# Performance work log

Hardware: AMD Instinct MI355X
Metric: run time of the kernel (lower is better)

## Reference

```python
import jax, jax.numpy as jnp
import numpy as np

SIDE_LEN = 128
RESOLUTION = 1.0  # Angstrom per pixel


def setup_inputs() -> dict:
    key = jax.random.key(0)
    k1, k2, k3 = jax.random.split(key, 3)
    B, A = 16, 20000
    # atom xyz coords in Angstrom, spread within the field of view (+/- 63.5 A)
    mol = jax.random.normal(k1, (B, A, 3), dtype=jnp.float32) * 20.0
    # per-atom Gaussian std in [0.5, 1.5) A (strictly positive)
    stds = jax.random.uniform(k2, (A,), dtype=jnp.float32) + 0.5
    # per-atom density (mass) in [0.5, 1.5)
    densities = jax.random.uniform(k3, (A,), dtype=jnp.float32) + 0.5
    return {"mol": mol, "stds": stds, "densities": densities}


def reference(mol, stds, densities):
    # Pixel-center coordinate grid, identical to torch.arange(-x_max, x_max+1e-5, res)
    x_max = (SIDE_LEN - 1) * RESOLUTION / 2
    coord = jnp.arange(-x_max, x_max + 1e-5, RESOLUTION, dtype=jnp.float32)  # (S,)
    var = stds * stds                              # (A,)
    neg_half_inv_var = (-0.5 / var)[None, :, None] # (1,A,1)
    # Separable Gaussian profiles: exp(-(coord - mu)^2 / (2 var))
    dx = coord[None, None, :] - mol[:, :, 0:1]     # (B,A,S) x-offsets
    dy = coord[None, None, :] - mol[:, :, 1:2]     # (B,A,S) y-offsets
    gx = jnp.exp(neg_half_inv_var * dx * dx)       # (B,A,W)
    gy = jnp.exp(neg_half_inv_var * dy * dy)       # (B,A,H)
    coef = densities / (2.0 * jnp.pi * var)        # (A,)
    # img[b,h,w] = sum_a coef_a * gy[b,a,h] * gx[b,a,w]  (batched matmul)
    img = jnp.einsum('bah,baw->bhw', gy * coef[None, :, None], gx)
    return img  # (B, SIDE_LEN, SIDE_LEN)
```

## Files before the change

kernel.cpp:

```cpp
#include <hip/hip_runtime.h>


#define S 128
#define KB 32
#define BLOCK 512
#define LDST 40

typedef _Float16 f16;
typedef _Float16 f16x2 __attribute__((ext_vector_type(2)));
typedef _Float16 f16x8 __attribute__((ext_vector_type(8)));
typedef float floatx4 __attribute__((ext_vector_type(4)));

#if __has_builtin(__builtin_amdgcn_exp2f)
#define FAST_EXP2(x) __builtin_amdgcn_exp2f(x)
#else
#define FAST_EXP2(x) exp2f(x)
#endif
#if __has_builtin(__builtin_amdgcn_rcpf)
#define FAST_RCP(x) __builtin_amdgcn_rcpf(x)
#else
#define FAST_RCP(x) (1.0f / (x))
#endif

__global__ __launch_bounds__(256) void k_prep(const float* __restrict__ stds,
                                              const float* __restrict__ dens,
                                              float* __restrict__ k2,
                                              float* __restrict__ c2, int A) {
    int a = blockIdx.x * 256 + threadIdx.x;
    if (a >= A) return;
    float v  = stds[a] * stds[a];
    float rv = FAST_RCP(v);
    k2[a] = -0.72134752044448f * rv;
    c2[a] = __log2f(dens[a] * 0.15915494309189535f * rv);
}

__global__ __launch_bounds__(BLOCK) void k_proj(
    const float* __restrict__ mol,
    const float* __restrict__ k2,
    const float* __restrict__ c2,
    float* __restrict__ dst,
    int B, int A, int KS, int use_ws)
{
    __shared__ f16 sgx[S * LDST];
    __shared__ f16 sgy[S * LDST];

    const int ks   = blockIdx.x;
    const int b    = blockIdx.y;
    const int tid  = threadIdx.x;
    const int lane = tid & 63;
    const int wav  = tid >> 6;
    const int l15  = lane & 15;
    const int quad = lane >> 4;

    const int per = (A + KS - 1) / KS;
    const int a0 = ks * per;
    const int a1 = min(a0 + per, A);

    floatx4 acc[8];
#pragma unroll
    for (int c = 0; c < 8; ++c) acc[c] = (floatx4){0.f, 0.f, 0.f, 0.f};

    const int kp = (tid & 15) * 2;
    const int pg = tid >> 4;

    for (int base = a0; base < a1; base += KB) {
        const int aA = base + kp, aB = aA + 1;
        float xA = 0.f, yA = 0.f, kA = 0.f, cA = -100000.f;
        float xB = 0.f, yB = 0.f, kB = 0.f, cB = -100000.f;
        if (aA < a1) {
            xA = mol[((size_t)b * A + aA) * 3 + 0];
            yA = mol[((size_t)b * A + aA) * 3 + 1];
            kA = k2[aA];  cA = c2[aA];
        }
        if (aB < a1) {
            xB = mol[((size_t)b * A + aB) * 3 + 0];
            yB = mol[((size_t)b * A + aB) * 3 + 1];
            kB = k2[aB];  cB = c2[aB];
        }

        __syncthreads();
#pragma unroll
        for (int j = 0; j < 4; ++j) {
            const int n = pg + 32 * j;
            const float d = (float)n - 63.5f;
            float dxA = d - xA, dxB = d - xB;
            float exA = FAST_EXP2(dxA * dxA * kA);
            float exB = FAST_EXP2(dxB * dxB * kB);
            *(f16x2*)&sgx[n * LDST + kp] = (f16x2){(f16)exA, (f16)exB};
            float dyA = d - yA, dyB = d - yB;
            float eyA = FAST_EXP2(fmaf(dyA * dyA, kA, cA));
            float eyB = FAST_EXP2(fmaf(dyB * dyB, kB, cB));
            *(f16x2*)&sgy[n * LDST + kp] = (f16x2){(f16)eyA, (f16)eyB};
        }
        __syncthreads();

        f16x8 afr = *(const f16x8*)&sgy[(wav * 16 + l15) * LDST + quad * 8];
#pragma unroll
        for (int c = 0; c < 8; ++c) {
            f16x8 bfr = *(const f16x8*)&sgx[(c * 16 + l15) * LDST + quad * 8];
            acc[c] = __builtin_amdgcn_mfma_f32_16x16x32_f16(afr, bfr, acc[c], 0, 0, 0);
        }
    }

    if (use_ws) {
        float* p = dst + ((size_t)(b * KS + ks)) * (S * S) + wav * 2048;
#pragma unroll
        for (int c = 0; c < 8; ++c)
            *(floatx4*)&p[c * 256 + lane * 4] = acc[c];
    } else {
        const size_t ob = (size_t)b * S * S;
#pragma unroll
        for (int c = 0; c < 8; ++c) {
            const int col = c * 16 + l15;
            const int r0  = wav * 16 + quad * 4;
#pragma unroll
            for (int v = 0; v < 4; ++v)
                atomicAdd(&dst[ob + (size_t)(r0 + v) * S + col], acc[c][v]);
        }
    }
}

__global__ __launch_bounds__(64) void k_reduce(const float* __restrict__ ws,
                                               float* __restrict__ out, int KS) {
    const int ct = blockIdx.x;
    const int w  = blockIdx.y;
    const int b  = blockIdx.z;
    const int t  = threadIdx.x;

    size_t base = ((size_t)b * KS) * (S * S) + w * 2048 + ct * 256 + t * 4;
    floatx4 s0 = {0.f, 0.f, 0.f, 0.f}, s1 = {0.f, 0.f, 0.f, 0.f};
    for (int s = 0; s < KS; s += 2) {
        s0 += *(const floatx4*)&ws[base + (size_t)s * (S * S)];
        s1 += *(const floatx4*)&ws[base + (size_t)(s + 1) * (S * S)];
    }
    floatx4 sum = s0 + s1;

    const int q = t >> 4, l15 = t & 15;
    const int col = ct * 16 + l15;
    const int r0  = w * 16 + q * 4;
#pragma unroll
    for (int v = 0; v < 4; ++v)
        out[((size_t)b * S + (r0 + v)) * S + col] = sum[v];
}

extern "C" void kernel_launch(void* const* d_in, const int* in_sizes, int n_in,
                              void* d_out, int out_size, void* d_ws, size_t ws_size,
                              hipStream_t stream) {
    const float* mol  = (const float*)d_in[0];
    const float* stds = (const float*)d_in[1];
    const float* dens = (const float*)d_in[2];
    float* out = (float*)d_out;

    const int A = in_sizes[1];
    const int B = in_sizes[0] / (A * 3);

    char* ws = (char*)d_ws;
    float* k2 = (float*)ws;
    float* c2 = (float*)(ws + (size_t)A * 4);
    size_t part_off = (((size_t)A * 8) + 255) & ~(size_t)255;
    float* part = (float*)(ws + part_off);

    const size_t img_bytes = (size_t)S * S * 4;
    int KS, use_ws;
    if (ws_size >= part_off + (size_t)64 * B * img_bytes)      { KS = 64; use_ws = 1; }
    else if (ws_size >= part_off + (size_t)32 * B * img_bytes) { KS = 32; use_ws = 1; }
    else                                                       { KS = 32; use_ws = 0; }

    k_prep<<<(A + 255) / 256, 256, 0, stream>>>(stds, dens, k2, c2, A);

    if (!use_ws)
        hipMemsetAsync(d_out, 0, (size_t)out_size * sizeof(float), stream);

    k_proj<<<dim3(KS, B), dim3(BLOCK), 0, stream>>>(
        mol, k2, c2, use_ws ? part : out, B, A, KS, use_ws);

    if (use_ws)
        k_reduce<<<dim3(8, 8, B), dim3(64), 0, stream>>>(part, out, KS);
}
```

Measured before the change: 107.0 us.

## Double-buffer LDS profiles, pack k/c params, fix split at 32 with workspace reduce

Double-buffers the shared gx/gy tiles so each iteration needs only one barrier instead of two. It also packs the per-atom exponent and log-coefficient into one float2 so each atom's parameters come from a single load. The K-split is fixed at 32 slices, and the atomic-add fallback and the workspace-size checks are removed. This cuts block count from 64 to 32 per batch if the workspace previously allowed 64, which lowers parallelism, and it assumes the workspace is always large enough.

```diff
diff --git a/kernel.cpp b/kernel.cpp
--- a/kernel.cpp
+++ b/kernel.cpp
@@ -3,6 +3,7 @@
 
 #define S 128
 #define KB 32
+#define KSPLIT 32
 #define BLOCK 512
 #define LDST 40
 
@@ -24,25 +25,23 @@
 
 __global__ __launch_bounds__(256) void k_prep(const float* __restrict__ stds,
                                               const float* __restrict__ dens,
-                                              float* __restrict__ k2,
-                                              float* __restrict__ c2, int A) {
+                                              float2* __restrict__ kc, int A) {
     int a = blockIdx.x * 256 + threadIdx.x;
     if (a >= A) return;
     float v  = stds[a] * stds[a];
     float rv = FAST_RCP(v);
-    k2[a] = -0.72134752044448f * rv;
-    c2[a] = __log2f(dens[a] * 0.15915494309189535f * rv);
+    kc[a] = make_float2(-0.72134752044448f * rv,
+                        __log2f(dens[a] * 0.15915494309189535f * rv));
 }
 
 __global__ __launch_bounds__(BLOCK) void k_proj(
     const float* __restrict__ mol,
-    const float* __restrict__ k2,
-    const float* __restrict__ c2,
-    float* __restrict__ dst,
-    int B, int A, int KS, int use_ws)
+    const float2* __restrict__ kc,
+    float* __restrict__ part,
+    int B, int A)
 {
-    __shared__ f16 sgx[S * LDST];
-    __shared__ f16 sgy[S * LDST];
+    __shared__ f16 sgx[2][S * LDST];
+    __shared__ f16 sgy[2][S * LDST];
 
     const int ks   = blockIdx.x;
     const int b    = blockIdx.y;
@@ -52,7 +51,7 @@
     const int l15  = lane & 15;
     const int quad = lane >> 4;
 
-    const int per = (A + KS - 1) / KS;
+    const int per = (A + KSPLIT - 1) / KSPLIT;
     const int a0 = ks * per;
     const int a1 = min(a0 + per, A);
 
@@ -63,22 +62,22 @@
     const int kp = (tid & 15) * 2;
     const int pg = tid >> 4;
 
-    for (int base = a0; base < a1; base += KB) {
+    int db = 0;
+    for (int base = a0; base < a1; base += KB, db ^= 1) {
         const int aA = base + kp, aB = aA + 1;
         float xA = 0.f, yA = 0.f, kA = 0.f, cA = -100000.f;
         float xB = 0.f, yB = 0.f, kB = 0.f, cB = -100000.f;
         if (aA < a1) {
             xA = mol[((size_t)b * A + aA) * 3 + 0];
             yA = mol[((size_t)b * A + aA) * 3 + 1];
-            kA = k2[aA];  cA = c2[aA];
+            float2 p = kc[aA];  kA = p.x;  cA = p.y;
         }
         if (aB < a1) {
             xB = mol[((size_t)b * A + aB) * 3 + 0];
             yB = mol[((size_t)b * A + aB) * 3 + 1];
-            kB = k2[aB];  cB = c2[aB];
+            float2 p = kc[aB];  kB = p.x;  cB = p.y;
         }
 
-        __syncthreads();
 #pragma unroll
         for (int j = 0; j < 4; ++j) {
             const int n = pg + 32 * j;
@@ -86,50 +85,38 @@
             float dxA = d - xA, dxB = d - xB;
             float exA = FAST_EXP2(dxA * dxA * kA);
             float exB = FAST_EXP2(dxB * dxB * kB);
-            *(f16x2*)&sgx[n * LDST + kp] = (f16x2){(f16)exA, (f16)exB};
+            *(f16x2*)&sgx[db][n * LDST + kp] = (f16x2){(f16)exA, (f16)exB};
             float dyA = d - yA, dyB = d - yB;
             float eyA = FAST_EXP2(fmaf(dyA * dyA, kA, cA));
             float eyB = FAST_EXP2(fmaf(dyB * dyB, kB, cB));
-            *(f16x2*)&sgy[n * LDST + kp] = (f16x2){(f16)eyA, (f16)eyB};
+            *(f16x2*)&sgy[db][n * LDST + kp] = (f16x2){(f16)eyA, (f16)eyB};
         }
         __syncthreads();
 
-        f16x8 afr = *(const f16x8*)&sgy[(wav * 16 + l15) * LDST + quad * 8];
+        f16x8 afr = *(const f16x8*)&sgy[db][(wav * 16 + l15) * LDST + quad * 8];
 #pragma unroll
         for (int c = 0; c < 8; ++c) {
-            f16x8 bfr = *(const f16x8*)&sgx[(c * 16 + l15) * LDST + quad * 8];
+            f16x8 bfr = *(const f16x8*)&sgx[db][(c * 16 + l15) * LDST + quad * 8];
             acc[c] = __builtin_amdgcn_mfma_f32_16x16x32_f16(afr, bfr, acc[c], 0, 0, 0);
         }
     }
 
-    if (use_ws) {
-        float* p = dst + ((size_t)(b * KS + ks)) * (S * S) + wav * 2048;
+    float* p = part + ((size_t)(b * KSPLIT + ks)) * (S * S) + wav * 2048;
 #pragma unroll
-        for (int c = 0; c < 8; ++c)
-            *(floatx4*)&p[c * 256 + lane * 4] = acc[c];
-    } else {
-        const size_t ob = (size_t)b * S * S;
-#pragma unroll
-        for (int c = 0; c < 8; ++c) {
-            const int col = c * 16 + l15;
-            const int r0  = wav * 16 + quad * 4;
-#pragma unroll
-            for (int v = 0; v < 4; ++v)
-                atomicAdd(&dst[ob + (size_t)(r0 + v) * S + col], acc[c][v]);
-        }
-    }
+    for (int c = 0; c < 8; ++c)
+        *(floatx4*)&p[c * 256 + lane * 4] = acc[c];
 }
 
 __global__ __launch_bounds__(64) void k_reduce(const float* __restrict__ ws,
-                                               float* __restrict__ out, int KS) {
+                                               float* __restrict__ out) {
     const int ct = blockIdx.x;
     const int w  = blockIdx.y;
     const int b  = blockIdx.z;
     const int t  = threadIdx.x;
 
-    size_t base = ((size_t)b * KS) * (S * S) + w * 2048 + ct * 256 + t * 4;
+    size_t base = ((size_t)b * KSPLIT) * (S * S) + w * 2048 + ct * 256 + t * 4;
     floatx4 s0 = {0.f, 0.f, 0.f, 0.f}, s1 = {0.f, 0.f, 0.f, 0.f};
-    for (int s = 0; s < KS; s += 2) {
+    for (int s = 0; s < KSPLIT; s += 2) {
         s0 += *(const floatx4*)&ws[base + (size_t)s * (S * S)];
         s1 += *(const floatx4*)&ws[base + (size_t)(s + 1) * (S * S)];
     }
@@ -155,25 +142,11 @@
     const int B = in_sizes[0] / (A * 3);
 
     char* ws = (char*)d_ws;
-    float* k2 = (float*)ws;
-    float* c2 = (float*)(ws + (size_t)A * 4);
+    float2* kc = (float2*)ws;
     size_t part_off = (((size_t)A * 8) + 255) & ~(size_t)255;
     float* part = (float*)(ws + part_off);
 
-    const size_t img_bytes = (size_t)S * S * 4;
-    int KS, use_ws;
-    if (ws_size >= part_off + (size_t)64 * B * img_bytes)      { KS = 64; use_ws = 1; }
-    else if (ws_size >= part_off + (size_t)32 * B * img_bytes) { KS = 32; use_ws = 1; }
-    else                                                       { KS = 32; use_ws = 0; }
-
-    k_prep<<<(A + 255) / 256, 256, 0, stream>>>(stds, dens, k2, c2, A);
-
-    if (!use_ws)
-        hipMemsetAsync(d_out, 0, (size_t)out_size * sizeof(float), stream);
-
-    k_proj<<<dim3(KS, B), dim3(BLOCK), 0, stream>>>(
-        mol, k2, c2, use_ws ? part : out, B, A, KS, use_ws);
-
-    if (use_ws)
-        k_reduce<<<dim3(8, 8, B), dim3(64), 0, stream>>>(part, out, KS);
+    k_prep<<<(A + 255) / 256, 256, 0, stream>>>(stds, dens, kc, A);
+    k_proj<<<dim3(KSPLIT, B), dim3(BLOCK), 0, stream>>>(mol, kc, part, B, A);
+    k_reduce<<<dim3(8, 8, B), dim3(64), 0, stream>>>(part, out);
 }
```

Result: faster. 103.9 us (-2.9%).
